# Performance work log

Measured on AMD Instinct MI355X. Metric: run time of the kernel, lower is better.

## Reference

```python
import jax, jax.numpy as jnp
from jax import lax
import numpy as np

B, C, T, S = 128, 512, 512, 128
L = 2 * S + 1  # blank-extended label length


def _ext_labels(seq, blank):
    # Channel index for each extended-label position s: blank at even s, seq[(s-1)//2] at odd s.
    s = jnp.arange(L)
    l = jnp.maximum(0, (s - 1) // 2)
    return jnp.where(s % 2 == 0, blank, seq[l])


def _alpha_pass(probs, lab):
    # probs: [C, T] per-frame probabilities; lab: [L] extended label channel ids.
    # Faithful to compute_alpha(): per-frame renormalization (Rabiner scaling) and
    # start-window masking (s >= L - 2*(T - t)); entries beyond end = 2t+2 are
    # structurally exact zeros, so summing the full masked column equals the
    # original's windowed sum.
    s = jnp.arange(L)
    p_ext = probs[lab, :].T  # [T, L]
    lab_m2 = jnp.concatenate([jnp.full((2,), -1, lab.dtype), lab[:-2]])
    # s-2 transition allowed only at odd s with non-repeated label (s==1 handled by zero pad).
    mask2 = (s % 2 == 1) & (lab != lab_m2)

    a0 = jnp.zeros(L, probs.dtype).at[0].set(p_ext[0, 0]).at[1].set(p_ext[0, 1])
    c0 = a0.sum()
    a0 = jnp.where(c0 > 0, a0 / c0, a0)

    def step(a_prev, inp):
        t, p_t = inp
        start = jnp.maximum(0, L - 2 * (T - t))
        a1 = jnp.concatenate([jnp.zeros(1, a_prev.dtype), a_prev[:-1]])
        a2 = jnp.concatenate([jnp.zeros(2, a_prev.dtype), a_prev[:-2]])
        a_new = (a_prev + a1 + jnp.where(mask2, a2, 0.0)) * p_t
        a_new = jnp.where(s >= start, a_new, 0.0)
        c = a_new.sum()
        a_new = jnp.where(c > 0, a_new / c, a_new)
        return a_new, a_new

    _, rest = lax.scan(step, a0, (jnp.arange(1, T), p_ext[1:]))
    return jnp.concatenate([a0[None, :], rest], axis=0).T  # [L, T]


def _ctc_single(probs, seq, blank):
    lab = _ext_labels(seq, blank)
    a = _alpha_pass(probs, lab)  # alphas
    # betas: alpha pass on time-reversed probs and reversed labels, then flip both axes
    lab_r = _ext_labels(jnp.flip(seq), blank)
    b = jnp.flip(_alpha_pass(jnp.flip(probs, axis=1), lab_r), axis=(0, 1))
    ab = a * b  # [L, T]
    p_ext = probs[lab, :]  # [L, T]
    lh = (ab / p_ext).sum(0)  # [T]
    return -jnp.sum(jnp.log(lh))


def setup_inputs() -> dict:
    key = jax.random.key(0)
    k1, k2 = jax.random.split(key)
    logits = jax.random.normal(k1, (B, C, T), dtype=jnp.float32)
    params = jax.nn.softmax(logits, axis=1)  # module consumes probabilities
    seq = jax.random.randint(k2, (B, S), 1, C, dtype=jnp.int32)  # labels never equal blank=0
    lengths = jnp.full((B,), 4 * T, dtype=jnp.int32)  # lengths//4 == T == params time dim
    return {"params": params, "seq": seq, "lengths": lengths, "blank": 0}


def reference(params, seq, lengths, blank):
    # lengths//4 == T (static, equals params.shape[2]) for all samples by construction.
    losses = jax.vmap(lambda p, q: _ctc_single(p, q, blank))(params, seq)
    return jnp.sum(losses)
```

## Files before the change

kernel.cpp:

```cpp
#include <hip/hip_runtime.h>
#include <math.h>


#define BB 128
#define CC 512
#define TT 512
#define SS 128
#define LL 257
#define LPADH 260

typedef unsigned int  uint;
typedef unsigned short ushort;

template<int CTRL>
__device__ __forceinline__ float dpp0_f32(float x){
    int v = __builtin_bit_cast(int, x);
    int r = __builtin_amdgcn_update_dpp(0, v, CTRL, 0xF, 0xF, true);
    return __builtin_bit_cast(float, r);
}
__device__ __forceinline__ float shfl_up1_f32(float x){ return dpp0_f32<0x138>(x); }
__device__ __forceinline__ float red8f(float x){
    x += dpp0_f32<0x111>(x);
    x += dpp0_f32<0x112>(x);
    x += dpp0_f32<0x114>(x);
    return x;
}
__device__ __forceinline__ float tail3f(float x){
    x += dpp0_f32<0x118>(x);
    x += dpp0_f32<0x142>(x);
    x += dpp0_f32<0x143>(x);
    return x;
}
__device__ __forceinline__ float full64f(float x){ return tail3f(red8f(x)); }
__device__ __forceinline__ float readlane63_f32(float x){
    int v = __builtin_bit_cast(int, x);
    return __builtin_bit_cast(float, __builtin_amdgcn_readlane(v, 63));
}
__device__ __forceinline__ float pow2if(int e){
    return __builtin_bit_cast(float, (127 + e) << 23);
}
__device__ __forceinline__ uint pk_bf16(float lo, float hi){
    return (__builtin_bit_cast(uint, hi) & 0xFFFF0000u)
         | (__builtin_bit_cast(uint, lo) >> 16);
}
__device__ __forceinline__ float up_lo(uint u){ return __builtin_bit_cast(float, u << 16); }
__device__ __forceinline__ float up_hi(uint u){ return __builtin_bit_cast(float, u & 0xFFFF0000u); }
__device__ __forceinline__ float up_us(ushort u){ return __builtin_bit_cast(float, ((uint)u) << 16); }
template<int CTRL>
__device__ __forceinline__ double dpp0_f64(double x){
    int2 v = __builtin_bit_cast(int2, x);
    int2 r;
    r.x = __builtin_amdgcn_update_dpp(0, v.x, CTRL, 0xF, 0xF, true);
    r.y = __builtin_amdgcn_update_dpp(0, v.y, CTRL, 0xF, 0xF, true);
    return __builtin_bit_cast(double, r);
}
__device__ __forceinline__ double full64d(double x){
    x += dpp0_f64<0x111>(x); x += dpp0_f64<0x112>(x); x += dpp0_f64<0x114>(x);
    x += dpp0_f64<0x118>(x); x += dpp0_f64<0x142>(x); x += dpp0_f64<0x143>(x);
    return x;
}

template<bool REV>
__device__ __forceinline__ void scan_body(
    int b, int wv, int l, const float* __restrict__ P,
    const int* __restrict__ seqg, int blank,
    ushort* __restrict__ W, ushort* __restrict__ W4, int* __restrict__ Eb)
{
    __shared__ float4 st4[64];
    __shared__ float  st1[64];
    __shared__ float  scSh[1];

    const bool is63 = (l == 63);
    const float* Pb = P + (size_t)b * (CC*TT);
    const int* sq = seqg + b*SS;

    int r1, r3; float m1, m3;
    if (!REV) {
        r1 = sq[2*l]; r3 = sq[2*l+1];
        int ip = (l==0) ? 0 : (2*l-1);
        m1 = (l==0) ? 1.f : ((r1 != sq[ip]) ? 1.f : 0.f);
        m3 = (r3 != r1) ? 1.f : 0.f;
    } else {
        r1 = sq[SS-1-2*l]; r3 = sq[SS-2-2*l];
        int ip = (l==0) ? 0 : (SS-2*l);
        m1 = (l==0) ? 1.f : ((r1 != sq[ip]) ? 1.f : 0.f);
        m3 = (r3 != r1) ? 1.f : 0.f;
    }
    const float* pBp = Pb + (size_t)blank*TT;
    const float* p1p = Pb + (size_t)r1*TT;
    const float* p3p = Pb + (size_t)r3*TT;
    int* EbB = Eb + b*64;

    const int tm0=(4*l+769)>>1, tm1=(4*l+770)>>1, tm2=(4*l+771)>>1, tm3=(4*l+772)>>1;

    float a0=0.f,a1=0.f,a2=0.f,a3=0.f,a4=0.f;
    float scNext = 1.f, Sfull = 0.f;
    const float u0i = (l==0) ? 1.f : 0.f;
    float pbB[8], pb1[8], pb3[8];
    uint sbLo[8], sbHi[8]; float s4f[8];

#define LOADPG(gg)                                                          \
  { _Pragma("unroll")                                                       \
    for (int j=0;j<8;++j){                                                  \
      int pc = REV ? (TT-1-((gg)*8+j)) : ((gg)*8+j);                        \
      pbB[j]=pBp[pc]; pb1[j]=p1p[pc]; pb3[j]=p3p[pc];                       \
    } }

#define STEP(g, j, FIRSTF, MASKF)                                           \
  {                                                                         \
    const int i = (g)*8 + (j);                                              \
    float u0,u1,u2,u3,u4;                                                   \
    if (FIRSTF) { u0=u0i; u1=u0i; u2=0.f; u3=0.f; u4=0.f; }                 \
    else {                                                                  \
      float e3u = shfl_up1_f32(a3);                                         \
      u0 = a0 + e3u; u1 = (a1+a0) + m1*e3u; u2 = a2+a1;                     \
      u3 = (a3+a2) + m3*a1; u4 = a4+a3;                                     \
      if (MASKF) {                                                          \
        if (i >= tm0) u0 = 0.f;                                             \
        if (i >= tm1) u1 = 0.f;                                             \
        if (i >= tm2) u2 = 0.f;                                             \
        if (i >= tm3) u3 = 0.f;                                             \
      }                                                                     \
    }                                                                       \
    float pB=pbB[j], pq=pb1[j], pr=pb3[j];                                  \
    if ((j)==0) { pB*=scNext; pq*=scNext; pr*=scNext; }                     \
    float n0=u0*pB, n1=u1*pq, n2=u2*pB, n3=u3*pr, n4=u4*pB;                 \
    sbLo[j]=pk_bf16(n0,n1); sbHi[j]=pk_bf16(n2,n3); s4f[j]=n4;              \
    if ((j)==5) {                                                           \
      float part=(n0+n1)+(n2+n3); if (is63) part+=n4;                       \
      Sfull = full64f(part);                                                \
    }                                                                       \
    if ((j)==7) {                                                           \
      float Su = readlane63_f32(Sfull);                                     \
      int ex = (__builtin_bit_cast(int, Su) >> 23) & 0xFF;                  \
      int e = (ex==0) ? 0 : (ex-127);                                       \
      e = e < -120 ? -120 : (e > 120 ? 120 : e);                            \
      scNext = pow2if(-e);                                                  \
      if (REV && l==0 && (g)+1 < 64) EbB[(g)+1] = e;                        \
    }                                                                       \
    a0=n0; a1=n1; a2=n2; a3=n3; a4=n4;                                      \
  }

#define RGROUP(g, FIRSTF, MASKF)                                            \
    STEP(g,0,FIRSTF,MASKF) STEP(g,1,false,MASKF) STEP(g,2,false,MASKF)      \
    STEP(g,3,false,MASKF)  STEP(g,4,false,MASKF) STEP(g,5,false,MASKF)      \
    STEP(g,6,false,MASKF)  STEP(g,7,false,MASKF)

#define STOREROWS(gg)                                                       \
  {                                                                         \
    ushort* Ww = W + ((size_t)b*TT + (size_t)(gg)*8) * LPADH;               \
    _Pragma("unroll")                                                       \
    for (int j=0;j<8;++j)                                                   \
      *reinterpret_cast<uint2*>(Ww + (size_t)j*LPADH + 4*l)                 \
          = make_uint2(sbLo[j], sbHi[j]);                                   \
    if (is63) {                                                             \
      uint4 pk;                                                             \
      pk.x = pk_bf16(s4f[0], s4f[1]);                                       \
      pk.y = pk_bf16(s4f[2], s4f[3]);                                       \
      pk.z = pk_bf16(s4f[4], s4f[5]);                                       \
      pk.w = pk_bf16(s4f[6], s4f[7]);                                       \
      *reinterpret_cast<uint4*>(W4 + (size_t)b*TT + (size_t)(gg)*8) = pk;   \
    }                                                                       \
  }

    LOADPG(wv)

    for (int g = 0; g < 64; ++g) {
        if ((g & 1) == wv) {
            if (g > 0) {
                float4 v = st4[l];
                a0 = v.x; a1 = v.y; a2 = v.z; a3 = v.w;
                a4 = st1[l];
                scNext = scSh[0];
            }
            if (g == 0)      { RGROUP(0, true,  false) }
            else if (g < 48) { RGROUP(g, false, false) }
            else             { RGROUP(g, false, true ) }
            st4[l] = make_float4(a0, a1, a2, a3);
            st1[l] = a4;
            if (l == 0) scSh[0] = scNext;
        } else {
            if (g >= 1) STOREROWS(g-1)
            if (g >= 1 && g < 63) LOADPG(g+1)
        }
        __syncthreads();
    }
    if (wv == 1) STOREROWS(63)

#undef STEP
#undef RGROUP
#undef STOREROWS
#undef LOADPG
}

__global__ __launch_bounds__(128, 1)
void ctc_scan(const float* __restrict__ P, const int* __restrict__ seqg,
              const int* __restrict__ blankp, ushort* __restrict__ Wa,
              ushort* __restrict__ Wb, ushort* __restrict__ W4a,
              ushort* __restrict__ W4b, int* __restrict__ Eb)
{
    const int bx = blockIdx.x;
    const int wv = threadIdx.x >> 6, l = threadIdx.x & 63;
    const int blank = blankp[0];
    if (bx < BB) scan_body<false>(bx,      wv, l, P, seqg, blank, Wa, W4a, Eb);
    else         scan_body<true >(bx - BB, wv, l, P, seqg, blank, Wb, W4b, Eb);
}

__global__ __launch_bounds__(64)
void ctc_combine(const ushort* __restrict__ Wa, const ushort* __restrict__ Wb,
                 const ushort* __restrict__ W4a, const ushort* __restrict__ W4b,
                 const int* __restrict__ Eb, const int* __restrict__ seqg,
                 double* __restrict__ Lq)
{
    const int b = blockIdx.x, q = blockIdx.y, l = threadIdx.x;
    const bool is63 = (l == 63);
    const int* sq = seqg + b*SS;
    const int r1 = sq[SS-1-2*l], r3 = sq[SS-2-2*l];
    const int ip = (l==0) ? 0 : (SS-2*l);
    const float m1 = (l==0) ? 1.f : ((r1 != sq[ip]) ? 1.f : 0.f);
    const float m3 = (r3 != r1) ? 1.f : 0.f;
    const int tm0=(4*l+769)>>1, tm1=(4*l+770)>>1, tm2=(4*l+771)>>1, tm3=(4*l+772)>>1;

    const ushort* WaB = Wa + (size_t)b*TT*LPADH;
    const ushort* WbB = Wb + (size_t)b*TT*LPADH;
    const ushort* W4aB = W4a + (size_t)b*TT;
    const ushort* W4bB = W4b + (size_t)b*TT;
    const int t0 = q*8;

    float Rcur;
    {
        const ushort* rw = WbB + (size_t)(TT-1-t0)*LPADH;
        uint2 xu = *reinterpret_cast<const uint2*>(rw + 4*l);
        float rnp = (up_lo(xu.x)+up_hi(xu.x))+(up_lo(xu.y)+up_hi(xu.y));
        if (is63) rnp += up_us(W4bB[TT-1-t0]);
        Rcur = full64f(rnp);
    }

    float PmN = 1.f, PmD = 1.f;
    int   Ei  = 0;

    #pragma unroll
    for (int k=0; k<8; ++k) {
        const int t = t0 + k;
        const int i = TT-1-t;
        const ushort* arow = WaB + (size_t)t*LPADH;
        uint2 au = *reinterpret_cast<const uint2*>(arow + (252 - 4*l));
        float av0 = up_lo(au.x), av1 = up_hi(au.x);
        float av2 = up_lo(au.y), av3 = up_hi(au.y);
        float a256 = up_us(W4aB[t]);
        float ar4 = shfl_up1_f32(av0);
        if (l == 0) ar4 = a256;

        float u0,u1,u2,u3,u4, rnext = 0.f;
        if (i > 0) {
            const ushort* rw = WbB + (size_t)(i-1)*LPADH;
            uint2 bu = *reinterpret_cast<const uint2*>(rw + 4*l);
            float bv0 = up_lo(bu.x), bv1 = up_hi(bu.x);
            float bv2 = up_lo(bu.y), bv3 = up_hi(bu.y);
            float b4 = up_us(W4bB[i-1]);
            float e3u = shfl_up1_f32(bv3);
            u0 = bv0 + e3u;
            u1 = (bv1 + bv0) + m1*e3u;
            u2 = bv2 + bv1;
            u3 = (bv3 + bv2) + m3*bv1;
            u4 = b4 + bv3;
            if (i >= TT - SS) {
                if (i >= tm0) u0 = 0.f;
                if (i >= tm1) u1 = 0.f;
                if (i >= tm2) u2 = 0.f;
                if (i >= tm3) u3 = 0.f;
            }
            rnext = (bv0+bv1)+(bv2+bv3);
            if (is63) rnext += b4;
        } else {
            u0 = (l==0)?1.f:0.f; u1 = u0; u2=0.f; u3=0.f; u4=0.f;
        }
        float trp = ar4*u0 + av3*u1 + av2*u2 + av1*u3;
        if (is63) trp += av0*u4;
        float sap = (av1 + av2) + (av3 + ar4);
        if (is63) sap += av0;

        float D  = full64f(trp);
        float S  = full64f(sap);
        float Rn = full64f(rnext);
        if (is63) {
            float dd = fmaxf(D, 1e-37f);
            uint bn = __builtin_bit_cast(uint, dd);
            Ei += (int)((bn >> 23) & 0xFFu) - 127;
            PmN *= __builtin_bit_cast(float, (bn & 0x807FFFFFu) | (127u<<23));
            float sr = fmaxf(S * Rcur, 1e-37f);
            uint bd = __builtin_bit_cast(uint, sr);
            Ei -= (int)((bd >> 23) & 0xFFu) - 127;
            PmD *= __builtin_bit_cast(float, (bd & 0x807FFFFFu) | (127u<<23));
            if (i > 0 && (i & 7) == 0) Ei -= Eb[b*64 + (i>>3)];
        }
        Rcur = Rn;
    }
    if (is63)
        Lq[b*64 + q] = log((double)PmN / (double)PmD) + (double)Ei * M_LN2;
}

__global__ __launch_bounds__(256)
void ctc_final(const double* __restrict__ Lq, float* __restrict__ out)
{
    const int t = threadIdx.x;
    double v = 0.0;
    #pragma unroll
    for (int k=0;k<32;++k) v += Lq[t + 256*k];
    double s = full64d(v);
    __shared__ double w[4];
    if ((t & 63) == 63) w[t>>6] = s;
    __syncthreads();
    if (t == 0) out[0] = (float)(-(w[0]+w[1]+w[2]+w[3]));
}

extern "C" void kernel_launch(void* const* d_in, const int* in_sizes, int n_in,
                              void* d_out, int out_size, void* d_ws, size_t ws_size,
                              hipStream_t stream)
{
    const float* P     = (const float*)d_in[0];
    const int*   seq   = (const int*)  d_in[1];
    const int*   blank = (const int*)  d_in[3];

    ushort* Wa  = (ushort*)d_ws;
    ushort* Wb  = Wa  + (size_t)BB*TT*LPADH;
    ushort* W4a = Wb  + (size_t)BB*TT*LPADH;
    ushort* W4b = W4a + (size_t)BB*TT;
    double* Lq  = (double*)(W4b + (size_t)BB*TT);
    int*    Eb  = (int*)(Lq + (size_t)BB*64);
    (void)ws_size; (void)in_sizes; (void)n_in; (void)out_size;

    ctc_scan<<<2*BB, 128, 0, stream>>>(P, seq, blank, Wa, Wb, W4a, W4b, Eb);
    ctc_combine<<<dim3(BB, 64), 64, 0, stream>>>(Wa, Wb, W4a, W4b, Eb, seq, Lq);
    ctc_final<<<1, 256, 0, stream>>>(Lq, (float*)d_out);
}
```

Measured before the change: 65.18 us.

## Double the ping-pong chunk to 16 timesteps with float4 probability loads

The two-wave ping-pong scan now advances 16 time steps per handoff instead of 8. This halves the number of __syncthreads barriers and the shared-memory state exchanges. Probability loads switch from scalar reads to float4 vector loads, with component selection adjusted for the reversed direction. The cost is more registers for the larger staging buffers, and the sequential recurrence length per wave turn doubles.

Result: faster. 62.10 us (-4.7%).

```diff
diff --git a/kernel.cpp b/kernel.cpp
--- a/kernel.cpp
+++ b/kernel.cpp
@@ -96,19 +96,24 @@
     float a0=0.f,a1=0.f,a2=0.f,a3=0.f,a4=0.f;
     float scNext = 1.f, Sfull = 0.f;
     const float u0i = (l==0) ? 1.f : 0.f;
-    float pbB[8], pb1[8], pb3[8];
-    uint sbLo[8], sbHi[8]; float s4f[8];
-
-#define LOADPG(gg)                                                          \
-  { _Pragma("unroll")                                                       \
-    for (int j=0;j<8;++j){                                                  \
-      int pc = REV ? (TT-1-((gg)*8+j)) : ((gg)*8+j);                        \
-      pbB[j]=pBp[pc]; pb1[j]=p1p[pc]; pb3[j]=p3p[pc];                       \
+    float4 qB[4], q1[4], q3[4];
+    uint sbLo[16], sbHi[16]; float s4f[16];
+
+#define COMP4(v,c) ((c)==0?(v).x:((c)==1?(v).y:((c)==2?(v).z:(v).w)))
+
+#define LOADPG2(ss)                                                         \
+  { const int base_ = REV ? (TT - 16*(ss) - 4) : (16*(ss));                 \
+    _Pragma("unroll")                                                       \
+    for (int k=0;k<4;++k){                                                  \
+      int c_ = REV ? (base_ - 4*k) : (base_ + 4*k);                         \
+      qB[k] = *reinterpret_cast<const float4*>(pBp + c_);                   \
+      q1[k] = *reinterpret_cast<const float4*>(p1p + c_);                   \
+      q3[k] = *reinterpret_cast<const float4*>(p3p + c_);                   \
     } }
 
-#define STEP(g, j, FIRSTF, MASKF)                                           \
+#define STEP16(ss, j, FIRSTF, MASKF)                                        \
   {                                                                         \
-    const int i = (g)*8 + (j);                                              \
+    const int i = 16*(ss) + (j);                                            \
     float u0,u1,u2,u3,u4;                                                   \
     if (FIRSTF) { u0=u0i; u1=u0i; u2=0.f; u3=0.f; u4=0.f; }                 \
     else {                                                                  \
@@ -122,75 +127,88 @@
         if (i >= tm3) u3 = 0.f;                                             \
       }                                                                     \
     }                                                                       \
-    float pB=pbB[j], pq=pb1[j], pr=pb3[j];                                  \
-    if ((j)==0) { pB*=scNext; pq*=scNext; pr*=scNext; }                     \
+    constexpr int ch_ = (j) >> 2;                                           \
+    constexpr int cm_ = REV ? ((3-(j)) & 3) : ((j) & 3);                    \
+    float pB = COMP4(qB[ch_], cm_);                                         \
+    float pq = COMP4(q1[ch_], cm_);                                         \
+    float pr = COMP4(q3[ch_], cm_);                                         \
+    if (((j)&7)==0) { pB*=scNext; pq*=scNext; pr*=scNext; }                 \
     float n0=u0*pB, n1=u1*pq, n2=u2*pB, n3=u3*pr, n4=u4*pB;                 \
     sbLo[j]=pk_bf16(n0,n1); sbHi[j]=pk_bf16(n2,n3); s4f[j]=n4;              \
-    if ((j)==5) {                                                           \
+    if (((j)&7)==5) {                                                       \
       float part=(n0+n1)+(n2+n3); if (is63) part+=n4;                       \
       Sfull = full64f(part);                                                \
     }                                                                       \
-    if ((j)==7) {                                                           \
+    if (((j)&7)==7) {                                                       \
       float Su = readlane63_f32(Sfull);                                     \
       int ex = (__builtin_bit_cast(int, Su) >> 23) & 0xFF;                  \
       int e = (ex==0) ? 0 : (ex-127);                                       \
       e = e < -120 ? -120 : (e > 120 ? 120 : e);                            \
       scNext = pow2if(-e);                                                  \
-      if (REV && l==0 && (g)+1 < 64) EbB[(g)+1] = e;                        \
+      const int g_ = i >> 3;                                                \
+      if (REV && l==0 && g_+1 < 64) EbB[g_+1] = e;                          \
     }                                                                       \
     a0=n0; a1=n1; a2=n2; a3=n3; a4=n4;                                      \
   }
 
-#define RGROUP(g, FIRSTF, MASKF)                                            \
-    STEP(g,0,FIRSTF,MASKF) STEP(g,1,false,MASKF) STEP(g,2,false,MASKF)      \
-    STEP(g,3,false,MASKF)  STEP(g,4,false,MASKF) STEP(g,5,false,MASKF)      \
-    STEP(g,6,false,MASKF)  STEP(g,7,false,MASKF)
-
-#define STOREROWS(gg)                                                       \
+#define RG2(ss, FIRSTF, MASKF)                                              \
+    STEP16(ss,0,FIRSTF,MASKF) STEP16(ss,1,false,MASKF)                      \
+    STEP16(ss,2,false,MASKF)  STEP16(ss,3,false,MASKF)                      \
+    STEP16(ss,4,false,MASKF)  STEP16(ss,5,false,MASKF)                      \
+    STEP16(ss,6,false,MASKF)  STEP16(ss,7,false,MASKF)                      \
+    STEP16(ss,8,false,MASKF)  STEP16(ss,9,false,MASKF)                      \
+    STEP16(ss,10,false,MASKF) STEP16(ss,11,false,MASKF)                     \
+    STEP16(ss,12,false,MASKF) STEP16(ss,13,false,MASKF)                     \
+    STEP16(ss,14,false,MASKF) STEP16(ss,15,false,MASKF)
+
+#define STOREROWS2(ss)                                                      \
   {                                                                         \
-    ushort* Ww = W + ((size_t)b*TT + (size_t)(gg)*8) * LPADH;               \
+    ushort* Ww = W + ((size_t)b*TT + (size_t)(ss)*16) * LPADH;              \
     _Pragma("unroll")                                                       \
-    for (int j=0;j<8;++j)                                                   \
+    for (int j=0;j<16;++j)                                                  \
       *reinterpret_cast<uint2*>(Ww + (size_t)j*LPADH + 4*l)                 \
           = make_uint2(sbLo[j], sbHi[j]);                                   \
     if (is63) {                                                             \
-      uint4 pk;                                                             \
-      pk.x = pk_bf16(s4f[0], s4f[1]);                                       \
-      pk.y = pk_bf16(s4f[2], s4f[3]);                                       \
-      pk.z = pk_bf16(s4f[4], s4f[5]);                                       \
-      pk.w = pk_bf16(s4f[6], s4f[7]);                                       \
-      *reinterpret_cast<uint4*>(W4 + (size_t)b*TT + (size_t)(gg)*8) = pk;   \
+      uint4 pk0, pk1;                                                       \
+      pk0.x = pk_bf16(s4f[0], s4f[1]);   pk0.y = pk_bf16(s4f[2], s4f[3]);   \
+      pk0.z = pk_bf16(s4f[4], s4f[5]);   pk0.w = pk_bf16(s4f[6], s4f[7]);   \
+      pk1.x = pk_bf16(s4f[8], s4f[9]);   pk1.y = pk_bf16(s4f[10], s4f[11]); \
+      pk1.z = pk_bf16(s4f[12], s4f[13]); pk1.w = pk_bf16(s4f[14], s4f[15]); \
+      ushort* w4p = W4 + (size_t)b*TT + (size_t)(ss)*16;                    \
+      *reinterpret_cast<uint4*>(w4p)     = pk0;                             \
+      *reinterpret_cast<uint4*>(w4p + 8) = pk1;                             \
     }                                                                       \
   }
 
-    LOADPG(wv)
-
-    for (int g = 0; g < 64; ++g) {
-        if ((g & 1) == wv) {
-            if (g > 0) {
+    LOADPG2(wv)
+
+    for (int s = 0; s < 32; ++s) {
+        if ((s & 1) == wv) {
+            if (s > 0) {
                 float4 v = st4[l];
                 a0 = v.x; a1 = v.y; a2 = v.z; a3 = v.w;
                 a4 = st1[l];
                 scNext = scSh[0];
             }
-            if (g == 0)      { RGROUP(0, true,  false) }
-            else if (g < 48) { RGROUP(g, false, false) }
-            else             { RGROUP(g, false, true ) }
+            if (s == 0)      { RG2(0, true,  false) }
+            else if (s < 24) { RG2(s, false, false) }
+            else             { RG2(s, false, true ) }
             st4[l] = make_float4(a0, a1, a2, a3);
             st1[l] = a4;
             if (l == 0) scSh[0] = scNext;
         } else {
-            if (g >= 1) STOREROWS(g-1)
-            if (g >= 1 && g < 63) LOADPG(g+1)
+            if (s >= 1) STOREROWS2(s-1)
+            if (s >= 1 && s < 31) LOADPG2(s+1)
         }
         __syncthreads();
     }
-    if (wv == 1) STOREROWS(63)
-
-#undef STEP
-#undef RGROUP
-#undef STOREROWS
-#undef LOADPG
+    if (wv == 1) STOREROWS2(31)
+
+#undef STEP16
+#undef RG2
+#undef STOREROWS2
+#undef LOADPG2
+#undef COMP4
 }
 
 __global__ __launch_bounds__(128, 1)
```
